# Kernel optimization log

Measured on AMD Instinct MI355X. Metric: run time of the kernel, lower is better.

## Reference

```python
import jax, jax.numpy as jnp
import numpy as np

BLOCK = (4, 4, 4)
NUM_HEADS = 8


def setup_inputs() -> dict:
    key = jax.random.key(0)
    ks = jax.random.split(key, 5)
    C = 128
    return {
        "x": jax.random.normal(ks[0], (2, C, 32, 62, 62), dtype=jnp.float32),
        "qkv_w": jax.random.normal(ks[1], (3 * C, C), dtype=jnp.float32) * 0.02,
        "qkv_b": jax.random.normal(ks[2], (3 * C,), dtype=jnp.float32) * 0.02,
        "conv_w": jax.random.normal(ks[3], (C, C, 1, 1, 1), dtype=jnp.float32) * 0.02,
        "conv_b": jax.random.normal(ks[4], (C,), dtype=jnp.float32) * 0.02,
    }


def reference(x, qkv_w, qkv_b, conv_w, conv_b):
    b0, b1, b2 = BLOCK
    heads = NUM_HEADS
    B, C, D, H0, W0 = x.shape
    pad_r = (-W0) % b2
    pad_b = (-H0) % b1
    x = jnp.pad(x, ((0, 0), (0, 0), (0, 0), (0, pad_b), (0, pad_r)))
    H, W = H0 + pad_b, W0 + pad_r
    d, h, w = D // b0, H // b1, W // b2
    hd = C // heads
    scale = hd ** (-0.5)
    T = b0 * b1 * b2  # tokens per 3D window
    nw = d * h * w    # number of windows

    # partition into windows: (B, nw, T, C)
    xw = x.reshape(B, C, d, b0, h, b1, w, b2).transpose(0, 2, 4, 6, 3, 5, 7, 1)
    xw = xw.reshape(B, nw, T, C)

    qkv = xw @ qkv_w.T + qkv_b  # (B, nw, T, 3C)
    qkv = qkv.reshape(B, nw, T, 3, heads, hd).transpose(3, 0, 1, 4, 2, 5)
    q, k, v = qkv[0], qkv[1], qkv[2]  # (B, nw, heads, T, hd)

    attn = jnp.einsum('bnhtc,bnhsc->bnhts', q, k) * scale

    if pad_r > 0 or pad_b > 0:
        mask = jnp.zeros((H, W), dtype=attn.dtype)
        if pad_b > 0:
            mask = mask.at[-pad_b:, :].set(1.0)
        if pad_r > 0:
            mask = mask.at[:, -pad_r:].set(1.0)
        # (h*w, b1*b2) per-2D-window pad flags
        mask = mask.reshape(h, b1, w, b2).transpose(0, 2, 1, 3).reshape(h * w, b1 * b2)
        am = mask[:, None, :] - mask[:, :, None]  # (h*w, b1*b2, b1*b2)
        am = jnp.where(am != 0, jnp.asarray(-1000.0, attn.dtype), jnp.asarray(0.0, attn.dtype))
        # tile over depth windows and depth tokens (matches torch .repeat)
        am = jnp.tile(am, (d, b0, b0))  # (nw, T, T)
        attn = attn + am[None, :, None, :, :]

    attn = jax.nn.softmax(attn, axis=-1)
    o = jnp.einsum('bnhts,bnhsc->bnhtc', attn, v)  # (B, nw, heads, T, hd)

    o = o.reshape(B, d, h, w, heads, b0, b1, b2, hd)
    o = o.transpose(0, 4, 8, 1, 5, 2, 6, 3, 7).reshape(B, C, D, H, W)
    o = o[:, :, :, :H0, :W0]

    # 1x1x1 Conv3d == channel mixing
    out = jnp.einsum('bcdhw,oc->bodhw', o, conv_w[:, :, 0, 0, 0])
    out = out + conv_b[None, :, None, None, None]
    return out
```

## Files before the change

kernel.cpp:

```cpp
#include <hip/hip_runtime.h>

typedef _Float16 f16x8 __attribute__((ext_vector_type(8)));
typedef _Float16 f16x4 __attribute__((ext_vector_type(4)));
typedef float    f32x4 __attribute__((ext_vector_type(4)));

__device__ __forceinline__ f32x4 mfma16(f16x8 a, f16x8 b, f32x4 c) {
  return __builtin_amdgcn_mfma_f32_16x16x32_f16(a, b, c, 0, 0, 0);
}

__global__ void cvt_weights(const float* __restrict__ qw, const float* __restrict__ cw,
                            _Float16* __restrict__ wq, _Float16* __restrict__ wc) {
  const int i = blockIdx.x * 256 + threadIdx.x;
  if (i < 384 * 128) wq[i] = (_Float16)qw[i];
  if (i < 128 * 128) wc[i] = (_Float16)cw[i];
}

__global__ void __launch_bounds__(256, 2)
win_attn(const float* __restrict__ xg, const _Float16* __restrict__ wq,
         const float* __restrict__ qb, const _Float16* __restrict__ wc,
         const float* __restrict__ cb, float* __restrict__ outg)
{
  __shared__ char xsm[16384];
  __shared__ char wsm[4][12288];

  const int tid  = threadIdx.x;
  const int lane = tid & 63;
  const int wv   = tid >> 6;
  const int l15  = lane & 15;
  const int g    = lane >> 4;

  const int raw = blockIdx.x;
  const int wid = ((raw & 7) << 9) | (raw >> 3);
  const int ww = wid & 15, hh = (wid >> 4) & 15, dd = (wid >> 8) & 7, bb = wid >> 11;

  const f32x4 fz = {0.f, 0.f, 0.f, 0.f};

  {
    const int m4 = lane & 3, q4 = lane >> 2;
    const int i0 = q4 >> 2, i1 = q4 & 3;
    const int z = dd * 4 + i0, y = hh * 4 + i1;
    const bool yv   = (y < 62);
    const bool full = (ww < 15);
    float va[8][4];
#pragma unroll
    for (int it = 0; it < 8; ++it) {
      const int c = wv * 32 + it * 4 + m4;
      const float* src = xg + (((size_t)(bb * 128 + c) * 32 + (size_t)z) * 3844
                               + (size_t)(y * 62 + ww * 4));
      float a0 = 0.f, a1 = 0.f, a2 = 0.f, a3 = 0.f;
      if (yv) {
        const float2 lo = *reinterpret_cast<const float2*>(src);
        a0 = lo.x; a1 = lo.y;
        if (full) {
          const float2 hi = *reinterpret_cast<const float2*>(src + 2);
          a2 = hi.x; a3 = hi.y;
        }
      }
      va[it][0] = a0; va[it][1] = a1; va[it][2] = a2; va[it][3] = a3;
    }
#pragma unroll
    for (int it = 0; it < 8; ++it) {
      float v0 = va[it][0], v1 = va[it][1], v2 = va[it][2], v3 = va[it][3];
      float t0 = __shfl_xor((m4 & 1) ? v0 : v1, 1);
      float t1 = __shfl_xor((m4 & 1) ? v2 : v3, 1);
      if (m4 & 1) { v0 = t0; v2 = t1; } else { v1 = t0; v3 = t1; }
      float t2 = __shfl_xor((m4 & 2) ? v0 : v2, 2);
      float t3 = __shfl_xor((m4 & 2) ? v1 : v3, 2);
      if (m4 & 2) { v0 = t2; v1 = t3; } else { v2 = t2; v3 = t3; }
      f16x4 pk; pk[0] = (_Float16)v0; pk[1] = (_Float16)v1;
                pk[2] = (_Float16)v2; pk[3] = (_Float16)v3;
      const int c0 = wv * 32 + it * 4;
      *reinterpret_cast<f16x4*>(xsm + ((lane * 256 + 2 * c0) ^ ((lane & 15) << 4))) = pk;
    }
  }
  __syncthreads();

  f32x4 acc[4][6];
#pragma unroll
  for (int i = 0; i < 4; ++i)
#pragma unroll
    for (int j = 0; j < 6; ++j) acc[i][j] = fz;

  const int swzA = l15 << 4;
#pragma unroll
  for (int kk = 0; kk < 4; ++kk) {
    f16x8 a[4];
#pragma unroll
    for (int ri = 0; ri < 4; ++ri)
      a[ri] = *reinterpret_cast<const f16x8*>(
          xsm + (ri * 16 + l15) * 256 + ((kk * 64 + g * 16) ^ swzA));
#pragma unroll
    for (int co = 0; co < 6; ++co) {
      const int col = (co >> 1) * 128 + wv * 32 + (co & 1) * 16 + l15;
      const f16x8 bfr = *reinterpret_cast<const f16x8*>(wq + col * 128 + kk * 32 + g * 8);
#pragma unroll
      for (int ri = 0; ri < 4; ++ri) acc[ri][co] = mfma16(a[ri], bfr, acc[ri][co]);
    }
  }
#pragma unroll
  for (int co = 0; co < 6; ++co) {
    const int col = (co >> 1) * 128 + wv * 32 + (co & 1) * 16 + l15;
    const float bias = qb[col];
    const float sc = (co < 2) ? 0.25f : 1.0f;
#pragma unroll
    for (int ri = 0; ri < 4; ++ri)
#pragma unroll
      for (int r = 0; r < 4; ++r) acc[ri][co][r] = (acc[ri][co][r] + bias) * sc;
  }
  __syncthreads();

  char* qkb = wsm[wv];
  char* Pb  = wsm[wv] + 4096;

  unsigned long long pm = 0ull;
  if (hh == 15) pm |= 0xFF00FF00FF00FF00ull;
  if (ww == 15) pm |= 0xCCCCCCCCCCCCCCCCull;

  const float LOG2E = 1.4426950408889634f;

#pragma unroll
  for (int hp = 0; hp < 2; ++hp) {
#pragma unroll
    for (int ri = 0; ri < 4; ++ri)
#pragma unroll
      for (int r = 0; r < 4; ++r) {
        const int t  = ri * 16 + g * 4 + r;
        const int sw = ((t >> 2) & 3) << 4;
        *reinterpret_cast<_Float16*>(qkb + t * 64 + ((2 * l15) ^ sw))        = (_Float16)acc[ri][hp][r];
        *reinterpret_cast<_Float16*>(qkb + t * 64 + ((32 + 2 * l15) ^ sw))   = (_Float16)acc[ri][2 + hp][r];
      }

    f16x8 ka[4], qa[4];
    const int swq = ((l15 >> 2) & 3) << 4;
#pragma unroll
    for (int ri = 0; ri < 4; ++ri) {
      f16x8 kz, qz;
      if (g < 2) {
        const int row = ri * 16 + l15;
        kz = *reinterpret_cast<const f16x8*>(qkb + row * 64 + ((32 + g * 16) ^ swq));
        qz = *reinterpret_cast<const f16x8*>(qkb + row * 64 + ((g * 16) ^ swq));
      } else {
#pragma unroll
        for (int e = 0; e < 8; ++e) { kz[e] = (_Float16)0.f; qz[e] = (_Float16)0.f; }
      }
      ka[ri] = kz; qa[ri] = qz;
    }
    f32x4 st[4][4];
#pragma unroll
    for (int ri = 0; ri < 4; ++ri)
#pragma unroll
      for (int cj = 0; cj < 4; ++cj) st[ri][cj] = mfma16(ka[ri], qa[cj], fz);

    if (pm) {
#pragma unroll
      for (int cj = 0; cj < 4; ++cj) {
        const int t = cj * 16 + l15;
        const unsigned ft = (unsigned)(pm >> t) & 1u;
#pragma unroll
        for (int ri = 0; ri < 4; ++ri)
#pragma unroll
          for (int r = 0; r < 4; ++r) {
            const int s = ri * 16 + g * 4 + r;
            const unsigned fs = (unsigned)(pm >> s) & 1u;
            if (fs != ft) st[ri][cj][r] -= 1000.f;
          }
      }
    }

#pragma unroll
    for (int cj = 0; cj < 4; ++cj) {
      float mx = st[0][cj][0];
#pragma unroll
      for (int ri = 0; ri < 4; ++ri)
#pragma unroll
        for (int r = 0; r < 4; ++r) mx = fmaxf(mx, st[ri][cj][r]);
      mx = fmaxf(mx, __shfl_xor(mx, 16));
      mx = fmaxf(mx, __shfl_xor(mx, 32));
      float sum = 0.f;
#pragma unroll
      for (int ri = 0; ri < 4; ++ri)
#pragma unroll
        for (int r = 0; r < 4; ++r) {
          const float e = __builtin_amdgcn_exp2f((st[ri][cj][r] - mx) * LOG2E);
          st[ri][cj][r] = e; sum += e;
        }
      sum += __shfl_xor(sum, 16);
      sum += __shfl_xor(sum, 32);
      const float inv = __builtin_amdgcn_rcpf(sum);
#pragma unroll
      for (int ri = 0; ri < 4; ++ri)
#pragma unroll
        for (int r = 0; r < 4; ++r) st[ri][cj][r] *= inv;
    }

#pragma unroll
    for (int cj = 0; cj < 4; ++cj) {
      const int t   = cj * 16 + l15;
      const int swp = (t & 7) << 4;
#pragma unroll
      for (int ri = 0; ri < 4; ++ri) {
        f16x4 pk; pk[0] = (_Float16)st[ri][cj][0]; pk[1] = (_Float16)st[ri][cj][1];
                  pk[2] = (_Float16)st[ri][cj][2]; pk[3] = (_Float16)st[ri][cj][3];
        *reinterpret_cast<f16x4*>(Pb + t * 128 + ((ri * 32 + g * 8) ^ swp)) = pk;
      }
    }
    {
      const int swv = (l15 & 7) << 4;
#pragma unroll
      for (int ri = 0; ri < 4; ++ri) {
        f16x4 pk; pk[0] = (_Float16)acc[ri][4 + hp][0]; pk[1] = (_Float16)acc[ri][4 + hp][1];
                  pk[2] = (_Float16)acc[ri][4 + hp][2]; pk[3] = (_Float16)acc[ri][4 + hp][3];
        *reinterpret_cast<f16x4*>(qkb + l15 * 128 + ((ri * 32 + g * 8) ^ swv)) = pk;
      }
    }

    f32x4 oacc[4];
#pragma unroll
    for (int ri = 0; ri < 4; ++ri) oacc[ri] = fz;
    const int swp2 = (l15 & 7) << 4;
#pragma unroll
    for (int k2 = 0; k2 < 2; ++k2) {
      const f16x8 pb = *reinterpret_cast<const f16x8*>(
          qkb + l15 * 128 + ((k2 * 64 + g * 16) ^ swp2));
#pragma unroll
      for (int ri = 0; ri < 4; ++ri) {
        const f16x8 pa = *reinterpret_cast<const f16x8*>(
            Pb + (ri * 16 + l15) * 128 + ((k2 * 64 + g * 16) ^ swp2));
        oacc[ri] = mfma16(pa, pb, oacc[ri]);
      }
    }
    const int ch = (2 * wv + hp) * 16 + l15;
#pragma unroll
    for (int ri = 0; ri < 4; ++ri)
#pragma unroll
      for (int r = 0; r < 4; ++r) {
        const int t = ri * 16 + g * 4 + r;
        *reinterpret_cast<_Float16*>(xsm + t * 256 + ((2 * ch) ^ ((t & 15) << 4)))
            = (_Float16)oacc[ri][r];
      }
  }
  __syncthreads();

  f32x4 cacc[4][2];
#pragma unroll
  for (int i = 0; i < 4; ++i) { cacc[i][0] = fz; cacc[i][1] = fz; }
#pragma unroll
  for (int kk = 0; kk < 4; ++kk) {
    f16x8 a[4];
#pragma unroll
    for (int ri = 0; ri < 4; ++ri)
      a[ri] = *reinterpret_cast<const f16x8*>(
          xsm + (ri * 16 + l15) * 256 + ((kk * 64 + g * 16) ^ swzA));
#pragma unroll
    for (int co = 0; co < 2; ++co) {
      const int cout = wv * 32 + co * 16 + l15;
      const f16x8 bfr = *reinterpret_cast<const f16x8*>(wc + cout * 128 + kk * 32 + g * 8);
#pragma unroll
      for (int ri = 0; ri < 4; ++ri) cacc[ri][co] = mfma16(a[ri], bfr, cacc[ri][co]);
    }
  }
  const int y = hh * 4 + g;
  if (y < 62) {
#pragma unroll
    for (int co = 0; co < 2; ++co) {
      const int cout = wv * 32 + co * 16 + l15;
      const float bias = cb[cout];
#pragma unroll
      for (int ri = 0; ri < 4; ++ri) {
        const int z = dd * 4 + ri;
        float* dst = outg + (((size_t)(bb * 128 + cout) * 32 + (size_t)z) * 3844
                             + (size_t)(y * 62 + ww * 4));
        float2 lo; lo.x = cacc[ri][co][0] + bias; lo.y = cacc[ri][co][1] + bias;
        *reinterpret_cast<float2*>(dst) = lo;
        if (ww < 15) {
          float2 hi; hi.x = cacc[ri][co][2] + bias; hi.y = cacc[ri][co][3] + bias;
          *reinterpret_cast<float2*>(dst + 2) = hi;
        }
      }
    }
  }
}

extern "C" void kernel_launch(void* const* d_in, const int* in_sizes, int n_in,
                              void* d_out, int out_size, void* d_ws, size_t ws_size,
                              hipStream_t stream) {
  const float* x  = (const float*)d_in[0];
  const float* qw = (const float*)d_in[1];
  const float* qb = (const float*)d_in[2];
  const float* cw = (const float*)d_in[3];
  const float* cb = (const float*)d_in[4];
  float* out = (float*)d_out;

  if (ws_size < (size_t)(384 * 128 + 128 * 128) * sizeof(_Float16)) return;
  _Float16* wq = (_Float16*)d_ws;
  _Float16* wc = wq + 384 * 128;

  cvt_weights<<<192, 256, 0, stream>>>(qw, cw, wq, wc);
  win_attn<<<4096, 256, 0, stream>>>(x, wq, qb, wc, cb, out);
}
```

Before: 188.6 us.

## Restructure attention stage with K=16 MFMA, LDS transpose reads and shuffled V operands

Rewrites the per-head attention inner loop. QK^T now uses 16x16x16 MFMA fed by ds_read_b64_tr_b16 transposed LDS reads, which removes the half-zeroed K=32 operands. V is packed to fp16 in registers and passed to the PV matmul through cross-lane shuffles instead of being staged in LDS. The output is computed transposed so it can be written with packed 64-bit stores. Per-wave scratch LDS shrinks from 12KB to 4KB and launch bounds rise to 4 blocks per CU, which raises occupancy but adds register pressure, inline asm, and manual waitcnt handling.

```diff
diff --git a/kernel.cpp b/kernel.cpp
--- a/kernel.cpp
+++ b/kernel.cpp
@@ -2,11 +2,33 @@
 
 typedef _Float16 f16x8 __attribute__((ext_vector_type(8)));
 typedef _Float16 f16x4 __attribute__((ext_vector_type(4)));
+typedef __fp16   fp16x2 __attribute__((ext_vector_type(2)));
 typedef float    f32x4 __attribute__((ext_vector_type(4)));
-
-__device__ __forceinline__ f32x4 mfma16(f16x8 a, f16x8 b, f32x4 c) {
+typedef unsigned int u32x2 __attribute__((ext_vector_type(2)));
+
+__device__ __forceinline__ f32x4 mfma32(f16x8 a, f16x8 b, f32x4 c) {
   return __builtin_amdgcn_mfma_f32_16x16x32_f16(a, b, c, 0, 0, 0);
 }
+__device__ __forceinline__ f32x4 mfma16(f16x4 a, f16x4 b, f32x4 c) {
+#if __has_builtin(__builtin_amdgcn_mfma_f32_16x16x16f16)
+  return __builtin_amdgcn_mfma_f32_16x16x16f16(a, b, c, 0, 0, 0);
+#else
+  f32x4 d;
+  asm volatile("v_mfma_f32_16x16x16_f16 %0, %1, %2, %3"
+               : "=v"(d) : "v"(a), "v"(b), "v"(c));
+  return d;
+#endif
+}
+
+__device__ __forceinline__ unsigned pk2(float a, float b) {
+  union { fp16x2 h; unsigned u; } cv;
+  cv.h = __builtin_amdgcn_cvt_pkrtz(a, b);
+  return cv.u;
+}
+
+#define TR_READ(dst, addr, OFF) \
+  asm volatile("ds_read_b64_tr_b16 %0, %1 offset:" OFF \
+               : "=v"(dst) : "v"(addr) : "memory")
 
 __global__ void cvt_weights(const float* __restrict__ qw, const float* __restrict__ cw,
                             _Float16* __restrict__ wq, _Float16* __restrict__ wc) {
@@ -15,13 +37,13 @@
   if (i < 128 * 128) wc[i] = (_Float16)cw[i];
 }
 
-__global__ void __launch_bounds__(256, 2)
+__global__ void __launch_bounds__(256, 4)
 win_attn(const float* __restrict__ xg, const _Float16* __restrict__ wq,
-         const float* __restrict__ qb, const _Float16* __restrict__ wc,
+         const float* __restrict__ qbias, const _Float16* __restrict__ wc,
          const float* __restrict__ cb, float* __restrict__ outg)
 {
   __shared__ char xsm[16384];
-  __shared__ char wsm[4][12288];
+  __shared__ char wsm[4][4096];
 
   const int tid  = threadIdx.x;
   const int lane = tid & 63;
@@ -94,23 +116,32 @@
       const int col = (co >> 1) * 128 + wv * 32 + (co & 1) * 16 + l15;
       const f16x8 bfr = *reinterpret_cast<const f16x8*>(wq + col * 128 + kk * 32 + g * 8);
 #pragma unroll
-      for (int ri = 0; ri < 4; ++ri) acc[ri][co] = mfma16(a[ri], bfr, acc[ri][co]);
+      for (int ri = 0; ri < 4; ++ri) acc[ri][co] = mfma32(a[ri], bfr, acc[ri][co]);
     }
   }
 #pragma unroll
   for (int co = 0; co < 6; ++co) {
     const int col = (co >> 1) * 128 + wv * 32 + (co & 1) * 16 + l15;
-    const float bias = qb[col];
+    const float bias = qbias[col];
     const float sc = (co < 2) ? 0.25f : 1.0f;
 #pragma unroll
     for (int ri = 0; ri < 4; ++ri)
 #pragma unroll
       for (int r = 0; r < 4; ++r) acc[ri][co][r] = (acc[ri][co][r] + bias) * sc;
   }
+  unsigned vp[2][4][2];
+#pragma unroll
+  for (int hp = 0; hp < 2; ++hp)
+#pragma unroll
+    for (int ri = 0; ri < 4; ++ri) {
+      vp[hp][ri][0] = pk2(acc[ri][4 + hp][0], acc[ri][4 + hp][1]);
+      vp[hp][ri][1] = pk2(acc[ri][4 + hp][2], acc[ri][4 + hp][3]);
+    }
   __syncthreads();
 
-  char* qkb = wsm[wv];
-  char* Pb  = wsm[wv] + 4096;
+  char* sb = wsm[wv];
+  const unsigned sb32 = (unsigned)(unsigned long long)sb;
+  const unsigned trb  = sb32 + 8u * (unsigned)lane;
 
   unsigned long long pm = 0ull;
   if (hh == 15) pm |= 0xFF00FF00FF00FF00ull;
@@ -121,123 +152,124 @@
 #pragma unroll
   for (int hp = 0; hp < 2; ++hp) {
 #pragma unroll
-    for (int ri = 0; ri < 4; ++ri)
-#pragma unroll
-      for (int r = 0; r < 4; ++r) {
-        const int t  = ri * 16 + g * 4 + r;
-        const int sw = ((t >> 2) & 3) << 4;
-        *reinterpret_cast<_Float16*>(qkb + t * 64 + ((2 * l15) ^ sw))        = (_Float16)acc[ri][hp][r];
-        *reinterpret_cast<_Float16*>(qkb + t * 64 + ((32 + 2 * l15) ^ sw))   = (_Float16)acc[ri][2 + hp][r];
-      }
-
-    f16x8 ka[4], qa[4];
-    const int swq = ((l15 >> 2) & 3) << 4;
-#pragma unroll
     for (int ri = 0; ri < 4; ++ri) {
-      f16x8 kz, qz;
-      if (g < 2) {
-        const int row = ri * 16 + l15;
-        kz = *reinterpret_cast<const f16x8*>(qkb + row * 64 + ((32 + g * 16) ^ swq));
-        qz = *reinterpret_cast<const f16x8*>(qkb + row * 64 + ((g * 16) ^ swq));
-      } else {
-#pragma unroll
-        for (int e = 0; e < 8; ++e) { kz[e] = (_Float16)0.f; qz[e] = (_Float16)0.f; }
-      }
-      ka[ri] = kz; qa[ri] = qz;
-    }
+      const int off = ri * 512 + l15 * 32 + g * 8;
+      u32x2 kw, qw2;
+      kw[0]  = pk2(acc[ri][2 + hp][0], acc[ri][2 + hp][1]);
+      kw[1]  = pk2(acc[ri][2 + hp][2], acc[ri][2 + hp][3]);
+      qw2[0] = pk2(acc[ri][hp][0], acc[ri][hp][1]);
+      qw2[1] = pk2(acc[ri][hp][2], acc[ri][hp][3]);
+      *reinterpret_cast<u32x2*>(sb + off)        = kw;
+      *reinterpret_cast<u32x2*>(sb + 2048 + off) = qw2;
+    }
+    asm volatile("s_waitcnt lgkmcnt(0)" ::: "memory");
+
+    f16x4 ka[4], qa[4];
+    TR_READ(ka[0], trb, "0");
+    TR_READ(ka[1], trb, "512");
+    TR_READ(ka[2], trb, "1024");
+    TR_READ(ka[3], trb, "1536");
+    TR_READ(qa[0], trb, "2048");
+    TR_READ(qa[1], trb, "2560");
+    TR_READ(qa[2], trb, "3072");
+    TR_READ(qa[3], trb, "3584");
+    asm volatile("s_waitcnt lgkmcnt(0)" ::: "memory");
+    __builtin_amdgcn_sched_barrier(0);
+
     f32x4 st[4][4];
 #pragma unroll
-    for (int ri = 0; ri < 4; ++ri)
-#pragma unroll
-      for (int cj = 0; cj < 4; ++cj) st[ri][cj] = mfma16(ka[ri], qa[cj], fz);
+    for (int si = 0; si < 4; ++si)
+#pragma unroll
+      for (int tj = 0; tj < 4; ++tj) st[si][tj] = mfma16(ka[si], qa[tj], fz);
 
     if (pm) {
 #pragma unroll
-      for (int cj = 0; cj < 4; ++cj) {
-        const int t = cj * 16 + l15;
+      for (int tj = 0; tj < 4; ++tj) {
+        const int t = tj * 16 + l15;
         const unsigned ft = (unsigned)(pm >> t) & 1u;
 #pragma unroll
-        for (int ri = 0; ri < 4; ++ri)
+        for (int si = 0; si < 4; ++si)
 #pragma unroll
           for (int r = 0; r < 4; ++r) {
-            const int s = ri * 16 + g * 4 + r;
+            const int s = si * 16 + g * 4 + r;
             const unsigned fs = (unsigned)(pm >> s) & 1u;
-            if (fs != ft) st[ri][cj][r] -= 1000.f;
+            if (fs != ft) st[si][tj][r] -= 1000.f;
           }
       }
     }
 
 #pragma unroll
-    for (int cj = 0; cj < 4; ++cj) {
-      float mx = st[0][cj][0];
-#pragma unroll
-      for (int ri = 0; ri < 4; ++ri)
-#pragma unroll
-        for (int r = 0; r < 4; ++r) mx = fmaxf(mx, st[ri][cj][r]);
+    for (int tj = 0; tj < 4; ++tj) {
+      float mx = st[0][tj][0];
+#pragma unroll
+      for (int si = 0; si < 4; ++si)
+#pragma unroll
+        for (int r = 0; r < 4; ++r) mx = fmaxf(mx, st[si][tj][r]);
       mx = fmaxf(mx, __shfl_xor(mx, 16));
       mx = fmaxf(mx, __shfl_xor(mx, 32));
       float sum = 0.f;
 #pragma unroll
-      for (int ri = 0; ri < 4; ++ri)
+      for (int si = 0; si < 4; ++si)
 #pragma unroll
         for (int r = 0; r < 4; ++r) {
-          const float e = __builtin_amdgcn_exp2f((st[ri][cj][r] - mx) * LOG2E);
-          st[ri][cj][r] = e; sum += e;
+          const float e = __builtin_amdgcn_exp2f((st[si][tj][r] - mx) * LOG2E);
+          st[si][tj][r] = e; sum += e;
         }
       sum += __shfl_xor(sum, 16);
       sum += __shfl_xor(sum, 32);
       const float inv = __builtin_amdgcn_rcpf(sum);
 #pragma unroll
-      for (int ri = 0; ri < 4; ++ri)
-#pragma unroll
-        for (int r = 0; r < 4; ++r) st[ri][cj][r] *= inv;
-    }
-
-#pragma unroll
-    for (int cj = 0; cj < 4; ++cj) {
-      const int t   = cj * 16 + l15;
-      const int swp = (t & 7) << 4;
-#pragma unroll
-      for (int ri = 0; ri < 4; ++ri) {
-        f16x4 pk; pk[0] = (_Float16)st[ri][cj][0]; pk[1] = (_Float16)st[ri][cj][1];
-                  pk[2] = (_Float16)st[ri][cj][2]; pk[3] = (_Float16)st[ri][cj][3];
-        *reinterpret_cast<f16x4*>(Pb + t * 128 + ((ri * 32 + g * 8) ^ swp)) = pk;
-      }
-    }
-    {
-      const int swv = (l15 & 7) << 4;
-#pragma unroll
-      for (int ri = 0; ri < 4; ++ri) {
-        f16x4 pk; pk[0] = (_Float16)acc[ri][4 + hp][0]; pk[1] = (_Float16)acc[ri][4 + hp][1];
-                  pk[2] = (_Float16)acc[ri][4 + hp][2]; pk[3] = (_Float16)acc[ri][4 + hp][3];
-        *reinterpret_cast<f16x4*>(qkb + l15 * 128 + ((ri * 32 + g * 8) ^ swv)) = pk;
-      }
-    }
-
-    f32x4 oacc[4];
-#pragma unroll
-    for (int ri = 0; ri < 4; ++ri) oacc[ri] = fz;
-    const int swp2 = (l15 & 7) << 4;
-#pragma unroll
-    for (int k2 = 0; k2 < 2; ++k2) {
-      const f16x8 pb = *reinterpret_cast<const f16x8*>(
-          qkb + l15 * 128 + ((k2 * 64 + g * 16) ^ swp2));
-#pragma unroll
-      for (int ri = 0; ri < 4; ++ri) {
+      for (int si = 0; si < 4; ++si)
+#pragma unroll
+        for (int r = 0; r < 4; ++r) st[si][tj][r] *= inv;
+    }
+
+    f32x4 oat[4] = {fz, fz, fz, fz};
+#pragma unroll
+    for (int kc = 0; kc < 2; ++kc) {
+#pragma unroll
+      for (int half = 0; half < 2; ++half) {
+        const int ri = 2 * kc + half;
+#pragma unroll
+        for (int tj = 0; tj < 4; ++tj) {
+          const int t = tj * 16 + l15;
+          u32x2 w;
+          w[0] = pk2(st[ri][tj][0], st[ri][tj][1]);
+          w[1] = pk2(st[ri][tj][2], st[ri][tj][3]);
+          *reinterpret_cast<u32x2*>(sb + t * 64 + ((half * 32 + g * 8) ^ ((t & 3) << 4))) = w;
+        }
+      }
+      const int srcA = l15 + 32 * (g & 1);
+      const unsigned a0 = __shfl(vp[hp][2 * kc][0], srcA);
+      const unsigned a1 = __shfl(vp[hp][2 * kc][1], srcA);
+      const unsigned a2 = __shfl(vp[hp][2 * kc][0], srcA + 16);
+      const unsigned a3 = __shfl(vp[hp][2 * kc][1], srcA + 16);
+      const unsigned b0 = __shfl(vp[hp][2 * kc + 1][0], srcA);
+      const unsigned b1 = __shfl(vp[hp][2 * kc + 1][1], srcA);
+      const unsigned b2 = __shfl(vp[hp][2 * kc + 1][0], srcA + 16);
+      const unsigned b3 = __shfl(vp[hp][2 * kc + 1][1], srcA + 16);
+      union { unsigned w[4]; f16x8 v; } av;
+      const bool hi = (g >= 2);
+      av.w[0] = hi ? b0 : a0; av.w[1] = hi ? b1 : a1;
+      av.w[2] = hi ? b2 : a2; av.w[3] = hi ? b3 : a3;
+#pragma unroll
+      for (int tj = 0; tj < 4; ++tj) {
+        const int t = tj * 16 + l15;
         const f16x8 pa = *reinterpret_cast<const f16x8*>(
-            Pb + (ri * 16 + l15) * 128 + ((k2 * 64 + g * 16) ^ swp2));
-        oacc[ri] = mfma16(pa, pb, oacc[ri]);
-      }
-    }
-    const int ch = (2 * wv + hp) * 16 + l15;
-#pragma unroll
-    for (int ri = 0; ri < 4; ++ri)
-#pragma unroll
-      for (int r = 0; r < 4; ++r) {
-        const int t = ri * 16 + g * 4 + r;
-        *reinterpret_cast<_Float16*>(xsm + t * 256 + ((2 * ch) ^ ((t & 15) << 4)))
-            = (_Float16)oacc[ri][r];
-      }
+            sb + t * 64 + ((g * 16) ^ ((t & 3) << 4)));
+        oat[tj] = mfma32(av.v, pa, oat[tj]);
+      }
+    }
+
+    const int h = 2 * wv + hp;
+#pragma unroll
+    for (int tj = 0; tj < 4; ++tj) {
+      const int t = tj * 16 + l15;
+      u32x2 w;
+      w[0] = pk2(oat[tj][0], oat[tj][1]);
+      w[1] = pk2(oat[tj][2], oat[tj][3]);
+      *reinterpret_cast<u32x2*>(xsm + t * 256 + ((h * 32 + g * 8) ^ ((t & 15) << 4))) = w;
+    }
   }
   __syncthreads();
 
@@ -256,7 +288,7 @@
       const int cout = wv * 32 + co * 16 + l15;
       const f16x8 bfr = *reinterpret_cast<const f16x8*>(wc + cout * 128 + kk * 32 + g * 8);
 #pragma unroll
-      for (int ri = 0; ri < 4; ++ri) cacc[ri][co] = mfma16(a[ri], bfr, cacc[ri][co]);
+      for (int ri = 0; ri < 4; ++ri) cacc[ri][co] = mfma32(a[ri], bfr, cacc[ri][co]);
     }
   }
   const int y = hh * 4 + g;
```

Result: slower. 365.6 us (+93.8%).
